# Performance work log

Hardware: AMD Instinct MI355X
Metric: run time of the kernel (lower is better)

The kernel has to match this reference:

```python
import jax, jax.numpy as jnp
import numpy as np

E = 640000   # number of scattered rows (edges)
N = 50000    # number of segments / attention keys
V = 128      # values_dim
K = 128      # keys_dim


def setup_inputs() -> dict:
    key = jax.random.key(0)
    k1, k2, k3, k4, k5 = jax.random.split(key, 5)
    scattered_values = jax.random.normal(k1, (E, V), dtype=jnp.float32)
    indices = jax.random.randint(k2, (E,), 0, N)
    attn_keys = jax.random.normal(k3, (N, K), dtype=jnp.float32)
    # nn.Linear(keys_dim, values_dim): weight [V, K], bias [V]
    lim = 1.0 / np.sqrt(K)
    W = jax.random.uniform(k4, (V, K), minval=-lim, maxval=lim, dtype=jnp.float32)
    b = jax.random.uniform(k5, (V,), minval=-lim, maxval=lim, dtype=jnp.float32)
    return {"scattered_values": scattered_values, "indices": indices,
            "attn_keys": attn_keys, "W": W, "b": b}


def reference(scattered_values, indices, attn_keys, W, b):
    # Project keys: [N, K] @ [K, V] + [V] -> [N, V]
    keys_proj = jnp.einsum('nk,vk->nv', attn_keys, W) + b
    # Gather projected key for each scattered row: [E, V]
    gathered = keys_proj[indices]
    # Per-row attention logit: [E]
    probs = jnp.sum(scattered_values * gathered, axis=1)
    # Segment (scatter) softmax over rows sharing the same index
    seg_max = jax.ops.segment_max(probs, indices, num_segments=N)
    ex = jnp.exp(probs - seg_max[indices])
    denom = jax.ops.segment_sum(ex, indices, num_segments=N)
    scores = ex / denom[indices]                      # [E]
    # Weighted segment-sum aggregation: [N, V]
    attn_applied = jax.ops.segment_sum(scattered_values * scores[:, None],
                                       indices, num_segments=N)
    return scores, attn_applied
```

## Files before the change

### kernel.cpp

```cpp
#include <hip/hip_runtime.h>
#include <cstdint>

#define DIM 128
#define CAP 64

__global__ __launch_bounds__(256) void hist_kernel(const int* __restrict__ idx,
                                                   int* __restrict__ count,
                                                   int* __restrict__ bucket,
                                                   int E) {
  int e = blockIdx.x * 256 + threadIdx.x;
  if (e >= E) return;
  int n = idx[e];
  int r = atomicAdd(&count[n], 1);
  if (r < CAP) bucket[n * CAP + r] = e;
}

__global__ __launch_bounds__(256) void keys_proj_gemm(const float* __restrict__ A,
                                                      const float* __restrict__ W,
                                                      const float* __restrict__ bias,
                                                      float* __restrict__ C,
                                                      int Nrows) {
  __shared__ float As[16][128];
  __shared__ float Ws[16][128];
  int t = threadIdx.x;
  int tx = t & 15;
  int ty = t >> 4;
  int n0 = blockIdx.x * 128;

  float acc[8][8];
#pragma unroll
  for (int r = 0; r < 8; ++r)
#pragma unroll
    for (int c = 0; c < 8; ++c) acc[r][c] = 0.f;

  for (int k0 = 0; k0 < DIM; k0 += 16) {
#pragma unroll
    for (int i = 0; i < 2; ++i) {
      int f = t + i * 256;
      int n = f >> 2;
      int kq = f & 3;
      int gn = n0 + n;
      if (gn >= Nrows) gn = Nrows - 1;
      const float4 a4 = *(const float4*)(A + (size_t)gn * DIM + k0 + kq * 4);
      As[kq * 4 + 0][n] = a4.x; As[kq * 4 + 1][n] = a4.y;
      As[kq * 4 + 2][n] = a4.z; As[kq * 4 + 3][n] = a4.w;
      const float4 w4 = *(const float4*)(W + (size_t)n * DIM + k0 + kq * 4);
      Ws[kq * 4 + 0][n] = w4.x; Ws[kq * 4 + 1][n] = w4.y;
      Ws[kq * 4 + 2][n] = w4.z; Ws[kq * 4 + 3][n] = w4.w;
    }
    __syncthreads();
#pragma unroll
    for (int kk = 0; kk < 16; ++kk) {
      float av[8], wv[8];
      *(float4*)&av[0] = *(const float4*)&As[kk][ty * 8];
      *(float4*)&av[4] = *(const float4*)&As[kk][ty * 8 + 4];
      *(float4*)&wv[0] = *(const float4*)&Ws[kk][tx * 8];
      *(float4*)&wv[4] = *(const float4*)&Ws[kk][tx * 8 + 4];
#pragma unroll
      for (int r = 0; r < 8; ++r)
#pragma unroll
        for (int c = 0; c < 8; ++c)
          acc[r][c] = fmaf(av[r], wv[c], acc[r][c]);
    }
    __syncthreads();
  }

#pragma unroll
  for (int r = 0; r < 8; ++r) {
    int gn = n0 + ty * 8 + r;
    if (gn < Nrows) {
#pragma unroll
      for (int c = 0; c < 8; c += 4) {
        int v = tx * 8 + c;
        float4 o;
        o.x = acc[r][c + 0] + bias[v + 0];
        o.y = acc[r][c + 1] + bias[v + 1];
        o.z = acc[r][c + 2] + bias[v + 2];
        o.w = acc[r][c + 3] + bias[v + 3];
        *(float4*)(C + (size_t)gn * DIM + v) = o;
      }
    }
  }
}

__global__ __launch_bounds__(256) void seg_attn_kernel(const float* __restrict__ sv,
                                                       const int* __restrict__ count,
                                                       const int* __restrict__ bucket,
                                                       const float* __restrict__ kp,
                                                       float* __restrict__ scores,
                                                       float* __restrict__ attn,
                                                       int Nseg) {
  int gw = (blockIdx.x * 256 + threadIdx.x) >> 6;
  int lane = threadIdx.x & 63;
  if (gw >= Nseg) return;
  int n = gw;
  int cnt = count[n];
  cnt = cnt > CAP ? CAP : cnt;

  float2 kp2 = *(const float2*)(kp + (size_t)n * DIM + lane * 2);

  int e_lane = (lane < cnt) ? bucket[n * CAP + lane] : 0;

  float p_lane = 0.f;
  float m = -3.4e38f;
  for (int i = 0; i < cnt; ++i) {
    int e = __shfl(e_lane, i);
    float2 s2 = *(const float2*)(sv + (size_t)e * DIM + lane * 2);
    float p = fmaf(s2.x, kp2.x, s2.y * kp2.y);
#pragma unroll
    for (int d = 1; d < 64; d <<= 1) p += __shfl_xor(p, d);
    if (lane == i) p_lane = p;
    m = fmaxf(m, p);
  }

  float ex = (lane < cnt) ? __expf(p_lane - m) : 0.f;
  float denom = ex;
#pragma unroll
  for (int d = 1; d < 64; d <<= 1) denom += __shfl_xor(denom, d);
  float sc = ex / denom;
  if (lane < cnt) scores[e_lane] = sc;

  float2 acc; acc.x = 0.f; acc.y = 0.f;
  for (int i = 0; i < cnt; ++i) {
    int e = __shfl(e_lane, i);
    float s = __shfl(sc, i);
    float2 s2 = *(const float2*)(sv + (size_t)e * DIM + lane * 2);
    acc.x = fmaf(s2.x, s, acc.x);
    acc.y = fmaf(s2.y, s, acc.y);
  }
  *(float2*)(attn + (size_t)n * DIM + lane * 2) = acc;
}

extern "C" void kernel_launch(void* const* d_in, const int* in_sizes, int n_in,
                              void* d_out, int out_size, void* d_ws, size_t ws_size,
                              hipStream_t stream) {
  const float* sv   = (const float*)d_in[0];
  const int*   idx  = (const int*)d_in[1];
  const float* A    = (const float*)d_in[2];
  const float* W    = (const float*)d_in[3];
  const float* bias = (const float*)d_in[4];

  const int E = in_sizes[1];
  const int N = in_sizes[2] / DIM;

  float* scores = (float*)d_out;
  float* attn   = (float*)d_out + E;

  char* ws = (char*)d_ws;
  size_t off_counts = 0;
  size_t off_bucket = ((size_t)N * 4 + 255) & ~(size_t)255;
  size_t off_kp     = off_bucket + (size_t)N * CAP * 4;
  int*   count  = (int*)(ws + off_counts);
  int*   bucket = (int*)(ws + off_bucket);
  float* kp     = (float*)(ws + off_kp);

  hipMemsetAsync(count, 0, (size_t)N * 4, stream);

  hist_kernel<<<(E + 255) / 256, 256, 0, stream>>>(idx, count, bucket, E);
  keys_proj_gemm<<<(N + 127) / 128, 256, 0, stream>>>(A, W, bias, kp, N);
  seg_attn_kernel<<<(N + 3) / 4, 256, 0, stream>>>(sv, count, bucket, kp,
                                                   scores, attn, N);
}
```

Baseline: 594.3 us.

## Process four edges per wavefront iteration with 16-lane float4 groups in segment attention

Segment attention now splits each 64-lane wavefront into four 16-lane groups. Each group handles one edge per iteration, using two float4 loads per lane instead of one float2 load across all 64 lanes. This cuts the serial per-edge loop iterations by about four times and shortens the dot-product shuffle reduction from 6 steps to 4. The segment max becomes a single wave-wide reduction after a lane remap, and the weighted aggregation ends with a cross-group shuffle reduction. The cost is extra shuffles at the end and some wasted loads from padded edges when the count is not a multiple of four.

```diff
diff --git a/kernel.cpp b/kernel.cpp
--- a/kernel.cpp
+++ b/kernel.cpp
@@ -96,23 +96,37 @@
   int n = gw;
   int cnt = count[n];
   cnt = cnt > CAP ? CAP : cnt;
+  int g = lane >> 4;
+  int q = lane & 15;
 
-  float2 kp2 = *(const float2*)(kp + (size_t)n * DIM + lane * 2);
+  const float4* kprow = (const float4*)(kp + (size_t)n * DIM);
+  float4 kpa = kprow[q * 2 + 0];
+  float4 kpb = kprow[q * 2 + 1];
 
   int e_lane = (lane < cnt) ? bucket[n * CAP + lane] : 0;
 
-  float p_lane = 0.f;
-  float m = -3.4e38f;
-  for (int i = 0; i < cnt; ++i) {
-    int e = __shfl(e_lane, i);
-    float2 s2 = *(const float2*)(sv + (size_t)e * DIM + lane * 2);
-    float p = fmaf(s2.x, kp2.x, s2.y * kp2.y);
+  int iters = (cnt + 3) >> 2;
+  float psave = 0.f;
+  for (int j = 0; j < iters; ++j) {
+    int ei = 4 * j + g;
+    int e = __shfl(e_lane, ei);
+    const float4* src = (const float4*)(sv + (size_t)e * DIM) + q * 2;
+    float4 a0 = src[0];
+    float4 a1 = src[1];
+    float d = a0.x * kpa.x + a0.y * kpa.y + a0.z * kpa.z + a0.w * kpa.w
+            + a1.x * kpb.x + a1.y * kpb.y + a1.z * kpb.z + a1.w * kpb.w;
+    d += __shfl_xor(d, 1);
+    d += __shfl_xor(d, 2);
+    d += __shfl_xor(d, 4);
+    d += __shfl_xor(d, 8);
+    if (q == j) psave = d;
+  }
+  float p_lane = __shfl(psave, (lane & 3) * 16 + (lane >> 2));
+  if (lane >= cnt) p_lane = -3.4e38f;
+
+  float m = p_lane;
 #pragma unroll
-    for (int d = 1; d < 64; d <<= 1) p += __shfl_xor(p, d);
-    if (lane == i) p_lane = p;
-    m = fmaxf(m, p);
-  }
-
+  for (int d = 1; d < 64; d <<= 1) m = fmaxf(m, __shfl_xor(m, d));
   float ex = (lane < cnt) ? __expf(p_lane - m) : 0.f;
   float denom = ex;
 #pragma unroll
@@ -120,15 +134,34 @@
   float sc = ex / denom;
   if (lane < cnt) scores[e_lane] = sc;
 
-  float2 acc; acc.x = 0.f; acc.y = 0.f;
-  for (int i = 0; i < cnt; ++i) {
-    int e = __shfl(e_lane, i);
-    float s = __shfl(sc, i);
-    float2 s2 = *(const float2*)(sv + (size_t)e * DIM + lane * 2);
-    acc.x = fmaf(s2.x, s, acc.x);
-    acc.y = fmaf(s2.y, s, acc.y);
+  float4 acc0 = {0.f, 0.f, 0.f, 0.f};
+  float4 acc1 = {0.f, 0.f, 0.f, 0.f};
+  for (int j = 0; j < iters; ++j) {
+    int ei = 4 * j + g;
+    int e = __shfl(e_lane, ei);
+    float s = __shfl(sc, ei);
+    const float4* src = (const float4*)(sv + (size_t)e * DIM) + q * 2;
+    float4 a0 = src[0];
+    float4 a1 = src[1];
+    acc0.x = fmaf(s, a0.x, acc0.x); acc0.y = fmaf(s, a0.y, acc0.y);
+    acc0.z = fmaf(s, a0.z, acc0.z); acc0.w = fmaf(s, a0.w, acc0.w);
+    acc1.x = fmaf(s, a1.x, acc1.x); acc1.y = fmaf(s, a1.y, acc1.y);
+    acc1.z = fmaf(s, a1.z, acc1.z); acc1.w = fmaf(s, a1.w, acc1.w);
   }
-  *(float2*)(attn + (size_t)n * DIM + lane * 2) = acc;
+  float* accf = (float*)&acc0;
+#pragma unroll
+  for (int mask = 16; mask < 64; mask <<= 1) {
+    acc0.x += __shfl_xor(acc0.x, mask); acc0.y += __shfl_xor(acc0.y, mask);
+    acc0.z += __shfl_xor(acc0.z, mask); acc0.w += __shfl_xor(acc0.w, mask);
+    acc1.x += __shfl_xor(acc1.x, mask); acc1.y += __shfl_xor(acc1.y, mask);
+    acc1.z += __shfl_xor(acc1.z, mask); acc1.w += __shfl_xor(acc1.w, mask);
+  }
+  (void)accf;
+  if (g == 0) {
+    float4* dst = (float4*)(attn + (size_t)n * DIM) + q * 2;
+    dst[0] = acc0;
+    dst[1] = acc1;
+  }
 }
 
 extern "C" void kernel_launch(void* const* d_in, const int* in_sizes, int n_in,
@@ -147,10 +180,9 @@
   float* attn   = (float*)d_out + E;
 
   char* ws = (char*)d_ws;
-  size_t off_counts = 0;
   size_t off_bucket = ((size_t)N * 4 + 255) & ~(size_t)255;
   size_t off_kp     = off_bucket + (size_t)N * CAP * 4;
-  int*   count  = (int*)(ws + off_counts);
+  int*   count  = (int*)ws;
   int*   bucket = (int*)(ws + off_bucket);
   float* kp     = (float*)(ws + off_kp);
 
```

New measurement: 545.9 us. -8.1%, faster.
